# Performance work log

Measured on AMD Instinct MI355X. Metric: run time of the kernel, lower is better.

The kernel has to match this reference:

```python
import jax, jax.numpy as jnp
import numpy as np

D_MODEL = 192
D_STATE = 16
D_CONV = 3
EXPAND = 2
D_INNER = EXPAND * D_MODEL
DT_RANK = (D_MODEL + 15) // 16  # ceil(d_model/16) = 12


def setup_inputs() -> dict:
    key = jax.random.key(0)
    ks = jax.random.split(key, 8)
    B, H, W = 4, 32, 32
    sc = lambda n: 1.0 / np.sqrt(n)
    x = jax.random.normal(ks[0], (B, H, W, D_MODEL), jnp.float32)
    W_in = jax.random.normal(ks[1], (D_MODEL, 2 * D_INNER), jnp.float32) * sc(D_MODEL)
    conv_w = jax.random.normal(ks[2], (D_INNER, 1, D_CONV, D_CONV), jnp.float32) * sc(D_CONV * D_CONV)
    conv_b = jnp.zeros((D_INNER,), jnp.float32)
    W_x = jax.random.normal(ks[3], (D_INNER, DT_RANK + 2 * D_STATE), jnp.float32) * sc(D_INNER)
    W_dt = jax.random.normal(ks[4], (DT_RANK, D_INNER), jnp.float32) * sc(DT_RANK)
    b_dt = jnp.zeros((D_INNER,), jnp.float32)
    A_log = jnp.log(jnp.tile(jnp.arange(1, D_STATE + 1, dtype=jnp.float32), (D_INNER, 1)))
    D_param = jnp.ones((D_INNER,), jnp.float32)
    W_out = jax.random.normal(ks[5], (D_INNER, D_MODEL), jnp.float32) * sc(D_INNER)
    gamma = jnp.ones((D_INNER,), jnp.float32)
    beta = jnp.zeros((D_INNER,), jnp.float32)
    return {"x": x, "W_in": W_in, "conv_w": conv_w, "conv_b": conv_b,
            "W_x": W_x, "W_dt": W_dt, "b_dt": b_dt, "A_log": A_log,
            "D_param": D_param, "W_out": W_out, "gamma": gamma, "beta": beta}


def _ssm_scan(u, W_x, W_dt, b_dt, A_log, D_param):
    # u: (B, L, D_inner). Log-cumsum closed-form linear SSM scan.
    x_dbl = u @ W_x                                   # (B,L,dt_rank+2N)
    dt = x_dbl[..., :DT_RANK]
    B_mat = x_dbl[..., DT_RANK:DT_RANK + D_STATE]     # (B,L,N)
    C_mat = x_dbl[..., DT_RANK + D_STATE:]            # (B,L,N)
    dt = jax.nn.softplus(dt @ W_dt + b_dt)            # (B,L,D)
    A = -jnp.exp(A_log)                               # (D,N)
    log_dA = jnp.einsum('bld,dn->bldn', dt, A)        # (B,L,D,N)
    dB_u = jnp.einsum('bld,bln->bldn', dt, B_mat) * u[..., None]
    log_decay = jnp.cumsum(log_dA, axis=1)
    decay = jnp.exp(log_decay)
    h = decay * jnp.cumsum(dB_u / (decay + 1e-12), axis=1)
    y = jnp.einsum('bldn,bln->bld', h, C_mat)
    return y + u * D_param


def reference(x, W_in, conv_w, conv_b, W_x, W_dt, b_dt, A_log, D_param, W_out, gamma, beta):
    B, H, W, C = x.shape
    xz = x @ W_in                                     # (B,H,W,2*D_inner)
    x_val, z = xz[..., :D_INNER], xz[..., D_INNER:]
    # depthwise 3x3 conv in NCHW
    xc = jnp.transpose(x_val, (0, 3, 1, 2))
    xc = jax.lax.conv_general_dilated(
        xc, conv_w, window_strides=(1, 1), padding='SAME',
        feature_group_count=D_INNER,
        dimension_numbers=('NCHW', 'OIHW', 'NCHW'))
    xc = xc + conv_b[None, :, None, None]
    xc = jax.nn.silu(xc)
    xv = jnp.transpose(xc, (0, 2, 3, 1))              # (B,H,W,D_inner)

    scan = lambda u: _ssm_scan(u, W_x, W_dt, b_dt, A_log, D_param)
    s1 = xv.reshape(B, H * W, D_INNER)                # row-major
    s2 = s1[:, ::-1]
    s3 = jnp.transpose(xv, (0, 2, 1, 3)).reshape(B, W * H, D_INNER)  # column-major
    s4 = s3[:, ::-1]
    y1 = scan(s1)
    y2 = scan(s2)[:, ::-1]
    y3 = scan(s3)
    y4 = scan(s4)[:, ::-1]
    # map column-major scans back to row-major order
    y3 = jnp.transpose(y3.reshape(B, W, H, D_INNER), (0, 2, 1, 3)).reshape(B, H * W, D_INNER)
    y4 = jnp.transpose(y4.reshape(B, W, H, D_INNER), (0, 2, 1, 3)).reshape(B, H * W, D_INNER)
    y = y1 + y2 + y3 + y4

    # LayerNorm over last dim (eps=1e-5)
    mu = jnp.mean(y, axis=-1, keepdims=True)
    var = jnp.mean(jnp.square(y - mu), axis=-1, keepdims=True)
    y = (y - mu) * jax.lax.rsqrt(var + 1e-5) * gamma + beta

    y = y.reshape(B, H, W, D_INNER) * jax.nn.silu(z)
    return y @ W_out
```

## Files before the change

kernel.cpp:

```cpp
#include <hip/hip_runtime.h>
#include <hip/hip_fp16.h>

#define DMODEL 192
#define DINNER 384
#define NPOS   4096
#define SEQL   1024
#define DSTATE 16
#define DTRANK 12

__device__ __forceinline__ float silu_f(float v) { return v * (1.f / (1.f + __expf(-v))); }

__device__ __forceinline__ int scan_pos(int dir, int l) {
    int s = (dir & 1) ? (SEQL - 1 - l) : l;
    return (dir & 2) ? (((s & 31) << 5) | (s >> 5)) : s;
}

__global__ void k1_inproj(const float* __restrict__ x, const float* __restrict__ W_in,
                          float* __restrict__ x_val, float* __restrict__ gz) {
    const int t = threadIdx.x;
    const int bi = blockIdx.x;
    const int colg = bi % 3;
    const int pos0 = (bi / 3) << 3;
    const int col = colg * 256 + t;

    const float* xr = x + pos0 * DMODEL;

    float acc[8] = {0,0,0,0,0,0,0,0};
    for (int c = 0; c < DMODEL; c += 4) {
        float w0 = W_in[(c + 0) * 768 + col];
        float w1 = W_in[(c + 1) * 768 + col];
        float w2 = W_in[(c + 2) * 768 + col];
        float w3 = W_in[(c + 3) * 768 + col];
#pragma unroll
        for (int g = 0; g < 8; ++g) {
            const float4 xv = *(const float4*)&xr[g * DMODEL + c];
            acc[g] += xv.x * w0 + xv.y * w1 + xv.z * w2 + xv.w * w3;
        }
    }
    if (col < DINNER) {
#pragma unroll
        for (int g = 0; g < 8; ++g) x_val[(pos0 + g) * DINNER + col] = acc[g];
    } else {
#pragma unroll
        for (int g = 0; g < 8; ++g) gz[(pos0 + g) * DINNER + (col - DINNER)] = silu_f(acc[g]);
    }
}

__global__ void k2_conv_dt(const float* __restrict__ x_val,
                           const float* __restrict__ conv_w, const float* __restrict__ conv_b,
                           const float* __restrict__ W_x, const float* __restrict__ W_dt,
                           const float* __restrict__ b_dt, const float* __restrict__ Dp,
                           __half* __restrict__ u_out, float* __restrict__ xd_out,
                           float* __restrict__ dt32, float* __restrict__ y_acc) {
    __shared__ float us[DINNER];
    __shared__ float part[8 * 44];
    __shared__ float xdl[44];
    const int t = threadIdx.x;
    const int pos = blockIdx.x;
    const int b = pos >> 10, hw = pos & 1023, h = hw >> 5, w = hw & 31;

    float acc = conv_b[t];
#pragma unroll
    for (int i = 0; i < 3; ++i) {
        int hh = h + i - 1;
        if (hh < 0 || hh > 31) continue;
#pragma unroll
        for (int j = 0; j < 3; ++j) {
            int ww = w + j - 1;
            if (ww < 0 || ww > 31) continue;
            acc += x_val[((b * 32 + hh) * 32 + ww) * DINNER + t] * conv_w[t * 9 + i * 3 + j];
        }
    }
    float uv = silu_f(acc);
    us[t] = uv;
    u_out[pos * DINNER + t] = __float2half(uv);
    __syncthreads();

    if (t < 352) {
        int o = t % 44, p = t / 44;
        float s = 0.f;
        int j0 = p * 48;
        for (int j = j0; j < j0 + 48; ++j) s += us[j] * W_x[j * 44 + o];
        part[p * 44 + o] = s;
    }
    __syncthreads();
    if (t < 44) {
        float s = 0.f;
#pragma unroll
        for (int p = 0; p < 8; ++p) s += part[p * 44 + t];
        xd_out[pos * 48 + t] = s;
        xdl[t] = s;
    }
    __syncthreads();

    float raw = b_dt[t];
#pragma unroll
    for (int r = 0; r < DTRANK; ++r) raw += xdl[r] * W_dt[r * DINNER + t];
    dt32[pos * DINNER + t] = fmaxf(raw, 0.f) + log1pf(__expf(-fabsf(raw)));

    y_acc[pos * DINNER + t] = 4.f * Dp[t] * uv;
}

__device__ __forceinline__ void k3_load(const float* __restrict__ dtb,
                                        const float* __restrict__ xb,
                                        const __half* __restrict__ ub,
                                        int dir, int l0, int d, int n,
                                        float* dtv, float* Bv, float* Cv, float* uv, int* pk) {
#pragma unroll
    for (int k = 0; k < 8; ++k) {
        int pos = scan_pos(dir, l0 + k);
        pk[k]  = pos;
        dtv[k] = dtb[pos * DINNER + d];
        Bv[k]  = xb[pos * 48 + DTRANK + n];
        Cv[k]  = xb[pos * 48 + DTRANK + DSTATE + n];
        uv[k]  = __half2float(ub[pos * DINNER + d]);
    }
}

__device__ __forceinline__ bool k3_compute(float A, float& cum, float& S,
                                           const float* dtv, const float* Bv,
                                           const float* Cv, const float* uv, const int* pk,
                                           float* __restrict__ yb, int d, int n) {
    float decay[8];
#pragma unroll
    for (int k = 0; k < 8; ++k) { cum += dtv[k] * A; decay[k] = __expf(cum); }
    float rc[8];
#pragma unroll
    for (int k = 0; k < 8; ++k) rc[k] = __builtin_amdgcn_rcpf(decay[k] + 1e-12f);
    float c[8];
#pragma unroll
    for (int k = 0; k < 8; ++k) {
        S += (dtv[k] * Bv[k] * uv[k]) * rc[k];
        c[k] = decay[k] * S * Cv[k];
    }
#pragma unroll
    for (int off = 1; off <= 8; off <<= 1) {
#pragma unroll
        for (int k = 0; k < 8; ++k) c[k] += __shfl_xor(c[k], off);
    }
    if (n == 0) {
#pragma unroll
        for (int k = 0; k < 8; ++k) atomicAdd(&yb[pk[k] * DINNER + d], c[k]);
    }
    return __ballot(cum > -110.f) != 0ull;
}

__global__ void k3_early(const __half* __restrict__ u, const float* __restrict__ xd,
                         const float* __restrict__ dt32, const float* __restrict__ A_log,
                         float* __restrict__ y_acc) {
    const int t = threadIdx.x;
    const int n = t & 15, dl = t >> 4;
    const int bi = blockIdx.x;
    const int chunk = bi % 24;
    const int b = (bi / 24) % 4;
    const int dir = bi / 96;
    const int d = chunk * 16 + dl;

    const float A = -__expf(A_log[d * DSTATE + n]);

    const __half* ub  = u    + b * SEQL * DINNER;
    const float* xb   = xd   + b * SEQL * 48;
    const float* dtb  = dt32 + b * SEQL * DINNER;
    float* yb = y_acc + b * SEQL * DINNER;

    float dtvA[8], BvA[8], CvA[8], uvA[8]; int pkA[8];
    float dtvB[8], BvB[8], CvB[8], uvB[8]; int pkB[8];

    float cum = 0.f, S = 0.f;
    k3_load(dtb, xb, ub, dir, 0, d, n, dtvA, BvA, CvA, uvA, pkA);
    for (int l0 = 0; l0 < SEQL; l0 += 16) {
        k3_load(dtb, xb, ub, dir, l0 + 8, d, n, dtvB, BvB, CvB, uvB, pkB);
        if (!k3_compute(A, cum, S, dtvA, BvA, CvA, uvA, pkA, yb, d, n)) break;
        int ln = (l0 + 16 < SEQL) ? (l0 + 16) : (l0 + 8);
        k3_load(dtb, xb, ub, dir, ln, d, n, dtvA, BvA, CvA, uvA, pkA);
        if (!k3_compute(A, cum, S, dtvB, BvB, CvB, uvB, pkB, yb, d, n)) break;
    }
}

__global__ void k4_out(const float* __restrict__ y_acc, const float* __restrict__ gz,
                       const float* __restrict__ gamma, const float* __restrict__ beta,
                       const float* __restrict__ W_out, float* __restrict__ out) {
    __shared__ float g_s[8 * DINNER];
    __shared__ float red[12];
    const int t = threadIdx.x;
    const int half = t / 192, tc = t % 192;
    const int lane = t & 63, wv = t >> 6;
    const int pos0 = blockIdx.x << 3;

    const float g0c = gamma[tc], g1c = gamma[tc + 192];
    const float b0c = beta[tc],  b1c = beta[tc + 192];

    for (int it = 0; it < 4; ++it) {
        int p = it * 2 + half;
        int pos = pos0 + p;
        float y0 = y_acc[pos * DINNER + tc];
        float y1 = y_acc[pos * DINNER + tc + 192];

        float s = y0 + y1;
#pragma unroll
        for (int off = 32; off > 0; off >>= 1) s += __shfl_xor(s, off);
        if (lane == 0) red[wv] = s;
        __syncthreads();
        float mu = (red[half * 3] + red[half * 3 + 1] + red[half * 3 + 2]) * (1.f / 384.f);

        float d0 = y0 - mu, d1 = y1 - mu;
        float sq = d0 * d0 + d1 * d1;
#pragma unroll
        for (int off = 32; off > 0; off >>= 1) sq += __shfl_xor(sq, off);
        if (lane == 0) red[6 + wv] = sq;
        __syncthreads();
        float var = (red[6 + half * 3] + red[6 + half * 3 + 1] + red[6 + half * 3 + 2]) * (1.f / 384.f);
        float inv = rsqrtf(var + 1e-5f);

        g_s[p * DINNER + tc]       = (d0 * inv * g0c + b0c) * gz[pos * DINNER + tc];
        g_s[p * DINNER + tc + 192] = (d1 * inv * g1c + b1c) * gz[pos * DINNER + tc + 192];
    }
    __syncthreads();

    float acc[4] = {0.f, 0.f, 0.f, 0.f};
    const int pbase = half * 4;
    for (int dd = 0; dd < DINNER; dd += 4) {
        float w0 = W_out[(dd + 0) * DMODEL + tc];
        float w1 = W_out[(dd + 1) * DMODEL + tc];
        float w2 = W_out[(dd + 2) * DMODEL + tc];
        float w3 = W_out[(dd + 3) * DMODEL + tc];
#pragma unroll
        for (int i = 0; i < 4; ++i) {
            const float4 g = *(const float4*)&g_s[(pbase + i) * DINNER + dd];
            acc[i] += g.x * w0 + g.y * w1 + g.z * w2 + g.w * w3;
        }
    }
#pragma unroll
    for (int i = 0; i < 4; ++i) out[(pos0 + pbase + i) * DMODEL + tc] = acc[i];
}

extern "C" void kernel_launch(void* const* d_in, const int* in_sizes, int n_in,
                              void* d_out, int out_size, void* d_ws, size_t ws_size,
                              hipStream_t stream) {
    (void)in_sizes; (void)n_in; (void)out_size; (void)ws_size;
    const float* x      = (const float*)d_in[0];
    const float* W_in   = (const float*)d_in[1];
    const float* conv_w = (const float*)d_in[2];
    const float* conv_b = (const float*)d_in[3];
    const float* W_x    = (const float*)d_in[4];
    const float* W_dt   = (const float*)d_in[5];
    const float* b_dt   = (const float*)d_in[6];
    const float* A_log  = (const float*)d_in[7];
    const float* Dp     = (const float*)d_in[8];
    const float* W_out  = (const float*)d_in[9];
    const float* gamma  = (const float*)d_in[10];
    const float* beta   = (const float*)d_in[11];

    char* base = (char*)d_ws;
    float*  x_val = (float*)base;
    __half* u     = (__half*)(base + 6291456);
    float*  xd    = (float*)(base + 9437184);
    float*  dt32  = (float*)(base + 10223616);
    float*  gz    = (float*)(base + 16515072);
    float*  y_acc = (float*)(base + 22806528);

    hipLaunchKernelGGL(k1_inproj, dim3(NPOS / 8 * 3), dim3(256), 0, stream, x, W_in, x_val, gz);
    hipLaunchKernelGGL(k2_conv_dt, dim3(NPOS), dim3(384), 0, stream,
                       x_val, conv_w, conv_b, W_x, W_dt, b_dt, Dp, u, xd, dt32, y_acc);
    hipLaunchKernelGGL(k3_early, dim3(384), dim3(256), 0, stream,
                       u, xd, dt32, A_log, y_acc);
    hipLaunchKernelGGL(k4_out, dim3(NPOS / 8), dim3(384), 0, stream,
                       y_acc, gz, gamma, beta, W_out, (float*)d_out);
}
```

Measured before the change: 214.8 us.

## Precompute dt prefix sums in separate kernels to break the scan's serial cumsum

Result: slower. 289.1 us (+34.6%).

```diff
diff --git a/kernel.cpp b/kernel.cpp
--- a/kernel.cpp
+++ b/kernel.cpp
@@ -9,11 +9,7 @@
 #define DTRANK 12
 
 __device__ __forceinline__ float silu_f(float v) { return v * (1.f / (1.f + __expf(-v))); }
-
-__device__ __forceinline__ int scan_pos(int dir, int l) {
-    int s = (dir & 1) ? (SEQL - 1 - l) : l;
-    return (dir & 2) ? (((s & 31) << 5) | (s >> 5)) : s;
-}
+__device__ __forceinline__ int swiz(int s) { return ((s & 31) << 5) | (s >> 5); }
 
 __global__ void k1_inproj(const float* __restrict__ x, const float* __restrict__ W_in,
                           float* __restrict__ x_val, float* __restrict__ gz) {
@@ -50,8 +46,8 @@
                            const float* __restrict__ conv_w, const float* __restrict__ conv_b,
                            const float* __restrict__ W_x, const float* __restrict__ W_dt,
                            const float* __restrict__ b_dt, const float* __restrict__ Dp,
-                           __half* __restrict__ u_out, float* __restrict__ xd_out,
-                           float* __restrict__ dt32, float* __restrict__ y_acc) {
+                           float* __restrict__ xd_out, float* __restrict__ dt32,
+                           float* __restrict__ du_out, float* __restrict__ y_acc) {
     __shared__ float us[DINNER];
     __shared__ float part[8 * 44];
     __shared__ float xdl[44];
@@ -73,7 +69,6 @@
     }
     float uv = silu_f(acc);
     us[t] = uv;
-    u_out[pos * DINNER + t] = __float2half(uv);
     __syncthreads();
 
     if (t < 352) {
@@ -96,58 +91,47 @@
     float raw = b_dt[t];
 #pragma unroll
     for (int r = 0; r < DTRANK; ++r) raw += xdl[r] * W_dt[r * DINNER + t];
-    dt32[pos * DINNER + t] = fmaxf(raw, 0.f) + log1pf(__expf(-fabsf(raw)));
-
-    y_acc[pos * DINNER + t] = 4.f * Dp[t] * uv;
-}
-
-__device__ __forceinline__ void k3_load(const float* __restrict__ dtb,
-                                        const float* __restrict__ xb,
-                                        const __half* __restrict__ ub,
-                                        int dir, int l0, int d, int n,
-                                        float* dtv, float* Bv, float* Cv, float* uv, int* pk) {
-#pragma unroll
-    for (int k = 0; k < 8; ++k) {
-        int pos = scan_pos(dir, l0 + k);
-        pk[k]  = pos;
-        dtv[k] = dtb[pos * DINNER + d];
-        Bv[k]  = xb[pos * 48 + DTRANK + n];
-        Cv[k]  = xb[pos * 48 + DTRANK + DSTATE + n];
-        uv[k]  = __half2float(ub[pos * DINNER + d]);
-    }
-}
-
-__device__ __forceinline__ bool k3_compute(float A, float& cum, float& S,
-                                           const float* dtv, const float* Bv,
-                                           const float* Cv, const float* uv, const int* pk,
-                                           float* __restrict__ yb, int d, int n) {
-    float decay[8];
-#pragma unroll
-    for (int k = 0; k < 8; ++k) { cum += dtv[k] * A; decay[k] = __expf(cum); }
-    float rc[8];
-#pragma unroll
-    for (int k = 0; k < 8; ++k) rc[k] = __builtin_amdgcn_rcpf(decay[k] + 1e-12f);
-    float c[8];
-#pragma unroll
-    for (int k = 0; k < 8; ++k) {
-        S += (dtv[k] * Bv[k] * uv[k]) * rc[k];
-        c[k] = decay[k] * S * Cv[k];
-    }
-#pragma unroll
-    for (int off = 1; off <= 8; off <<= 1) {
-#pragma unroll
-        for (int k = 0; k < 8; ++k) c[k] += __shfl_xor(c[k], off);
-    }
-    if (n == 0) {
-#pragma unroll
-        for (int k = 0; k < 8; ++k) atomicAdd(&yb[pk[k] * DINNER + d], c[k]);
-    }
-    return __ballot(cum > -110.f) != 0ull;
-}
-
-__global__ void k3_early(const __half* __restrict__ u, const float* __restrict__ xd,
-                         const float* __restrict__ dt32, const float* __restrict__ A_log,
-                         float* __restrict__ y_acc) {
+    float dtv = fmaxf(raw, 0.f) + log1pf(__expf(-fabsf(raw)));
+    dt32[pos * DINNER + t]   = dtv;
+    du_out[pos * DINNER + t] = dtv * uv;
+    y_acc[pos * DINNER + t]  = 4.f * Dp[t] * uv;
+}
+
+__global__ void k2pA(const float* __restrict__ dt32, float* __restrict__ tot) {
+    const int t = threadIdx.x;
+    const int bi = blockIdx.x;
+    const int c = bi & 7, b = (bi >> 3) & 3, o = bi >> 5;
+    const float* base = dt32 + b * SEQL * DINNER + t;
+    float s = 0.f;
+    for (int i = 0; i < 128; ++i) {
+        int l = c * 128 + i;
+        int pos = o ? swiz(l) : l;
+        s += base[pos * DINNER];
+    }
+    tot[((o * 4 + b) * 8 + c) * DINNER + t] = s;
+}
+
+__global__ void k2pB(const float* __restrict__ dt32, const float* __restrict__ tot,
+                     float* __restrict__ P0, float* __restrict__ P2) {
+    const int t = threadIdx.x;
+    const int bi = blockIdx.x;
+    const int c = bi & 7, b = (bi >> 3) & 3, o = bi >> 5;
+    float run = 0.f;
+    for (int cc = 0; cc < 8; ++cc)
+        if (cc < c) run += tot[((o * 4 + b) * 8 + cc) * DINNER + t];
+    const float* base = dt32 + b * SEQL * DINNER + t;
+    float* P = (o ? P2 : P0) + b * SEQL * DINNER + t;
+    for (int i = 0; i < 128; ++i) {
+        int l = c * 128 + i;
+        int pos = o ? swiz(l) : l;
+        run += base[pos * DINNER];
+        P[l * DINNER] = run;
+    }
+}
+
+__global__ void k3_scan(const float* __restrict__ du, const float* __restrict__ xd,
+                        const float* __restrict__ P0, const float* __restrict__ P2,
+                        const float* __restrict__ A_log, float* __restrict__ y_acc) {
     const int t = threadIdx.x;
     const int n = t & 15, dl = t >> 4;
     const int bi = blockIdx.x;
@@ -157,23 +141,50 @@
     const int d = chunk * 16 + dl;
 
     const float A = -__expf(A_log[d * DSTATE + n]);
-
-    const __half* ub  = u    + b * SEQL * DINNER;
-    const float* xb   = xd   + b * SEQL * 48;
-    const float* dtb  = dt32 + b * SEQL * DINNER;
+    const int fwd = !(dir & 1);
+
+    const float* Pb  = ((dir & 2) ? P2 : P0) + b * SEQL * DINNER + d;
+    const float  T   = Pb[(SEQL - 1) * DINNER];
+    const float* dub = du + b * SEQL * DINNER + d;
+    const float* xb  = xd + b * SEQL * 48;
     float* yb = y_acc + b * SEQL * DINNER;
 
-    float dtvA[8], BvA[8], CvA[8], uvA[8]; int pkA[8];
-    float dtvB[8], BvB[8], CvB[8], uvB[8]; int pkB[8];
-
-    float cum = 0.f, S = 0.f;
-    k3_load(dtb, xb, ub, dir, 0, d, n, dtvA, BvA, CvA, uvA, pkA);
-    for (int l0 = 0; l0 < SEQL; l0 += 16) {
-        k3_load(dtb, xb, ub, dir, l0 + 8, d, n, dtvB, BvB, CvB, uvB, pkB);
-        if (!k3_compute(A, cum, S, dtvA, BvA, CvA, uvA, pkA, yb, d, n)) break;
-        int ln = (l0 + 16 < SEQL) ? (l0 + 16) : (l0 + 8);
-        k3_load(dtb, xb, ub, dir, ln, d, n, dtvA, BvA, CvA, uvA, pkA);
-        if (!k3_compute(A, cum, S, dtvB, BvB, CvB, uvB, pkB, yb, d, n)) break;
+    float S = 0.f;
+    for (int l0 = 0; l0 < SEQL; l0 += 8) {
+        float cumv[8], duv[8], Bv[8], Cv[8];
+        int pk[8];
+#pragma unroll
+        for (int k = 0; k < 8; ++k) {
+            int l = l0 + k;
+            int s = fwd ? l : (SEQL - 1 - l);
+            int pos = (dir & 2) ? swiz(s) : s;
+            pk[k] = pos;
+            cumv[k] = fwd ? Pb[l * DINNER]
+                          : (l == SEQL - 1 ? T : T - Pb[(SEQL - 2 - l) * DINNER]);
+            duv[k] = dub[pos * DINNER];
+            Bv[k]  = xb[pos * 48 + DTRANK + n];
+            Cv[k]  = xb[pos * 48 + DTRANK + DSTATE + n];
+        }
+        float decay[8], rc[8], c[8];
+#pragma unroll
+        for (int k = 0; k < 8; ++k) decay[k] = __expf(A * cumv[k]);
+#pragma unroll
+        for (int k = 0; k < 8; ++k) rc[k] = __builtin_amdgcn_rcpf(decay[k] + 1e-12f);
+#pragma unroll
+        for (int k = 0; k < 8; ++k) {
+            S += (duv[k] * Bv[k]) * rc[k];
+            c[k] = decay[k] * S * Cv[k];
+        }
+#pragma unroll
+        for (int off = 1; off <= 8; off <<= 1) {
+#pragma unroll
+            for (int k = 0; k < 8; ++k) c[k] += __shfl_xor(c[k], off);
+        }
+        if (n == 0) {
+#pragma unroll
+            for (int k = 0; k < 8; ++k) atomicAdd(&yb[pk[k] * DINNER + d], c[k]);
+        }
+        if (__ballot(A * cumv[7] > -110.f) == 0ull) break;
     }
 }
 
@@ -252,18 +263,23 @@
     const float* beta   = (const float*)d_in[11];
 
     char* base = (char*)d_ws;
-    float*  x_val = (float*)base;
-    __half* u     = (__half*)(base + 6291456);
-    float*  xd    = (float*)(base + 9437184);
-    float*  dt32  = (float*)(base + 10223616);
-    float*  gz    = (float*)(base + 16515072);
-    float*  y_acc = (float*)(base + 22806528);
+    float* x_val = (float*)(base + 0);
+    float* xd    = (float*)(base + 6291456);
+    float* dt32  = (float*)(base + 7077888);
+    float* du    = (float*)(base + 13369344);
+    float* gz    = (float*)(base + 19660800);
+    float* y_acc = (float*)(base + 25952256);
+    float* P0    = (float*)(base + 32243712);
+    float* P2    = (float*)(base + 38535168);
+    float* tot   = (float*)(base + 44826624);
 
     hipLaunchKernelGGL(k1_inproj, dim3(NPOS / 8 * 3), dim3(256), 0, stream, x, W_in, x_val, gz);
     hipLaunchKernelGGL(k2_conv_dt, dim3(NPOS), dim3(384), 0, stream,
-                       x_val, conv_w, conv_b, W_x, W_dt, b_dt, Dp, u, xd, dt32, y_acc);
-    hipLaunchKernelGGL(k3_early, dim3(384), dim3(256), 0, stream,
-                       u, xd, dt32, A_log, y_acc);
+                       x_val, conv_w, conv_b, W_x, W_dt, b_dt, Dp, xd, dt32, du, y_acc);
+    hipLaunchKernelGGL(k2pA, dim3(64), dim3(384), 0, stream, dt32, tot);
+    hipLaunchKernelGGL(k2pB, dim3(64), dim3(384), 0, stream, dt32, tot, P0, P2);
+    hipLaunchKernelGGL(k3_scan, dim3(384), dim3(256), 0, stream,
+                       du, xd, P0, P2, A_log, y_acc);
     hipLaunchKernelGGL(k4_out, dim3(NPOS / 8), dim3(384), 0, stream,
                        y_acc, gz, gamma, beta, W_out, (float*)d_out);
 }
```
